# Kernel optimization log

Measured on AMD Instinct MI355X. Metric: run time of the kernel, lower is better.

Reference implementation:

```python
import jax, jax.numpy as jnp
import numpy as np

N_HEADS = 32
N_KV = 8
N_REP = N_HEADS // N_KV  # 4
HEAD_DIM = 128
DIM = 4096


def _rope(x, cos, sin, start_pos):
    # x: (B, H, T, hd); cos/sin: (max_seq, hd//2)
    T = x.shape[2]
    c = jax.lax.dynamic_slice_in_dim(cos, start_pos, T, axis=0)[None, None]  # (1,1,T,hd/2)
    s = jax.lax.dynamic_slice_in_dim(sin, start_pos, T, axis=0)[None, None]
    x1, x2 = x[..., : HEAD_DIM // 2], x[..., HEAD_DIM // 2:]
    return jnp.concatenate([x1 * c - x2 * s, x2 * c + x1 * s], axis=-1)


def setup_inputs() -> dict:
    key = jax.random.key(0)
    ks = jax.random.split(key, 7)
    B, T = 1, 2048
    sc = 0.02
    return {
        "x": jax.random.normal(ks[0], (B, T, DIM), jnp.float32),
        "cos": jax.random.normal(ks[1], (T, HEAD_DIM // 2), jnp.float32),
        "sin": jax.random.normal(ks[2], (T, HEAD_DIM // 2), jnp.float32),
        "wq": jax.random.normal(ks[3], (N_HEADS * HEAD_DIM, DIM), jnp.float32) * sc,
        "wk": jax.random.normal(ks[4], (N_KV * HEAD_DIM, DIM), jnp.float32) * sc,
        "wv": jax.random.normal(ks[5], (N_KV * HEAD_DIM, DIM), jnp.float32) * sc,
        "wo": jax.random.normal(ks[6], (DIM, DIM), jnp.float32) * sc,
        "start_pos": 0,
    }


def reference(x, cos, sin, wq, wk, wv, wo, start_pos):
    B, T, _ = x.shape
    # Projections (nn.Linear: y = x @ W^T)
    q = (x @ wq.T).reshape(B, T, N_HEADS, HEAD_DIM).transpose(0, 2, 1, 3)  # (B,Hq,T,hd)
    k = (x @ wk.T).reshape(B, T, N_KV, HEAD_DIM).transpose(0, 2, 1, 3)    # (B,Hk,T,hd)
    v = (x @ wv.T).reshape(B, T, N_KV, HEAD_DIM).transpose(0, 2, 1, 3)
    q = _rope(q, cos, sin, start_pos)
    k = _rope(k, cos, sin, start_pos)
    # GQA: group query heads per kv head instead of materializing repeat_kv
    qg = q.reshape(B, N_KV, N_REP, T, HEAD_DIM)
    scale = 1.0 / jnp.sqrt(jnp.float32(HEAD_DIM))
    scores = jnp.einsum('bgrqd,bgkd->bgrqk', qg, k) * scale  # (B,Hk,rep,T,T)
    causal = jnp.tril(jnp.ones((T, T), dtype=bool))
    scores = jnp.where(causal, scores, jnp.finfo(scores.dtype).min)
    attn = jax.nn.softmax(scores, axis=-1)
    yg = jnp.einsum('bgrqk,bgkd->bgrqd', attn, v)  # (B,Hk,rep,T,hd)
    y = yg.reshape(B, N_HEADS, T, HEAD_DIM).transpose(0, 2, 1, 3).reshape(B, T, DIM)
    return y @ wo.T
```

## Files before the change

### kernel.cpp

```cpp
#include <hip/hip_runtime.h>
#include <hip/hip_bf16.h>
#include <stdint.h>

using bf16 = __hip_bfloat16;
using bf16x8 = __attribute__((ext_vector_type(8))) short;
using f32x4  = __attribute__((ext_vector_type(4))) float;

#define AS1 __attribute__((address_space(1)))
#define AS3 __attribute__((address_space(3)))

__device__ __forceinline__ void async_ld16(const void* g, void* l) {
    __builtin_amdgcn_global_load_lds((const AS1 void*)g, (AS3 void*)l, 16, 0, 0);
}

__device__ __forceinline__ f32x4 mfma_bf16(bf16x8 a, bf16x8 b, f32x4 c) {
    return __builtin_amdgcn_mfma_f32_16x16x32_bf16(a, b, c, 0, 0, 0);
}

__device__ __forceinline__ float sexp(float x) {
    return __expf(fmaxf(x, -80.0f));
}

template<int N> __device__ __forceinline__ float dpp_max16(float x) {
    int xi = __builtin_bit_cast(int, x);
    int yi = __builtin_amdgcn_update_dpp(xi, xi, 0x110 | N, 0xf, 0xf, false);
    return fmaxf(x, __builtin_bit_cast(float, yi));
}
template<int N> __device__ __forceinline__ float dpp_add16(float x) {
    int xi = __builtin_bit_cast(int, x);
    int yi = __builtin_amdgcn_update_dpp(0, xi, 0x110 | N, 0xf, 0xf, true);
    return x + __builtin_bit_cast(float, yi);
}
__device__ __forceinline__ float bcast15(float x) {
    return __builtin_bit_cast(float,
        __builtin_amdgcn_ds_swizzle(__builtin_bit_cast(int, x), 0x01F0));
}
__device__ __forceinline__ float redmax16(float x) {
    x = dpp_max16<1>(x); x = dpp_max16<2>(x);
    x = dpp_max16<4>(x); x = dpp_max16<8>(x);
    return bcast15(x);
}
__device__ __forceinline__ float redsum16(float x) {
    x = dpp_add16<1>(x); x = dpp_add16<2>(x);
    x = dpp_add16<4>(x); x = dpp_add16<8>(x);
    return bcast15(x);
}

__device__ __forceinline__ void cvt8(const float* p, bf16* d) {
    float4 lo = *(const float4*)p;
    float4 hi = *(const float4*)(p + 4);
    bf16 t8[8] = {__float2bfloat16(lo.x), __float2bfloat16(lo.y),
                  __float2bfloat16(lo.z), __float2bfloat16(lo.w),
                  __float2bfloat16(hi.x), __float2bfloat16(hi.y),
                  __float2bfloat16(hi.z), __float2bfloat16(hi.w)};
    *(bf16x8*)d = *(const bf16x8*)t8;
}

__global__ __launch_bounds__(256) void cvt4_k(const float* __restrict__ x,  bf16* __restrict__ xb,
                                              const float* __restrict__ wq, bf16* __restrict__ wqb,
                                              const float* __restrict__ wk, bf16* __restrict__ wkb,
                                              const float* __restrict__ wv, bf16* __restrict__ wvb) {
    int stride = gridDim.x * blockDim.x;
    for (int u = blockIdx.x * blockDim.x + threadIdx.x; u < 4194304; u += stride) {
        const float* s; bf16* d; size_t off;
        if (u < 1048576)      { s = x;  d = xb;  off = (size_t)u * 8; }
        else if (u < 3145728) { s = wq; d = wqb; off = (size_t)(u - 1048576) * 8; }
        else if (u < 3670016) { s = wk; d = wkb; off = (size_t)(u - 3145728) * 8; }
        else                  { s = wv; d = wvb; off = (size_t)(u - 3670016) * 8; }
        cvt8(s + off, d + off);
    }
}

__global__ __launch_bounds__(256) void cvt_f32_bf16(const float* __restrict__ src,
                                                    bf16* __restrict__ dst, int n8) {
    int stride = gridDim.x * blockDim.x;
    for (int u = blockIdx.x * blockDim.x + threadIdx.x; u < n8; u += stride)
        cvt8(src + (size_t)u * 8, dst + (size_t)u * 8);
}

template<bool SRCF32>
__device__ __forceinline__ void stage_tile(const void* __restrict__ src,
                                           bf16* __restrict__ s,
                                           int row0, int K, int k0, int tid) {
    if constexpr (SRCF32) {
        const float* g = (const float*)src;
        #pragma unroll
        for (int i = 0; i < 2; ++i) {
            int u = tid + 256 * i;
            int row = u >> 2, c8 = (u & 3) * 8;
            cvt8(g + (size_t)(row0 + row) * K + k0 + c8, &s[row * 32 + c8]);
        }
    } else {
        const bf16* g = (const bf16*)src;
        const int wave = tid >> 6, lane = tid & 63;
        const int c0 = wave * 64 + lane;
        const int r0 = c0 >> 2, cb0 = (c0 & 3) * 16;
        const int c1 = 256 + c0;
        const int r1 = c1 >> 2, cb1 = (c1 & 3) * 16;
        async_ld16((const char*)(g + (size_t)(row0 + r0) * K + k0) + cb0,
                   (char*)s + wave * 1024);
        async_ld16((const char*)(g + (size_t)(row0 + r1) * K + k0) + cb1,
                   (char*)s + 4096 + wave * 1024);
    }
}

template<bool AF32, bool BF32, int MODE>
__global__ __launch_bounds__(256) void gemm_bt(const void* __restrict__ A,
                                               const void* __restrict__ B,
                                               void* __restrict__ C,
                                               bf16* __restrict__ Qp,
                                               bf16* __restrict__ Kp,
                                               bf16* __restrict__ Vp,
                                               int M, int N, int K) {
    __shared__ bf16 sA[128 * 32];
    __shared__ bf16 sB[128 * 32];
    const int tid  = threadIdx.x;
    const int lane = tid & 63;
    const int wave = tid >> 6;
    const int m0 = blockIdx.y * 128;
    const int n0 = blockIdx.x * 128;
    const int mrow = (wave >> 1) * 64;
    const int ncol = (wave & 1) * 64;

    f32x4 acc[4][4] = {};

    for (int k0 = 0; k0 < K; k0 += 32) {
        __syncthreads();
        stage_tile<AF32>(A, sA, m0, K, k0, tid);
        stage_tile<BF32>(B, sB, n0, K, k0, tid);
        __syncthreads();

        bf16x8 af[4], bfr[4];
        #pragma unroll
        for (int i = 0; i < 4; ++i)
            af[i] = *(const bf16x8*)&sA[(mrow + i * 16 + (lane & 15)) * 32 + (lane >> 4) * 8];
        #pragma unroll
        for (int j = 0; j < 4; ++j)
            bfr[j] = *(const bf16x8*)&sB[(ncol + j * 16 + (lane & 15)) * 32 + (lane >> 4) * 8];
        #pragma unroll
        for (int i = 0; i < 4; ++i)
            #pragma unroll
            for (int j = 0; j < 4; ++j)
                acc[i][j] = mfma_bf16(af[i], bfr[j], acc[i][j]);
    }

    #pragma unroll
    for (int i = 0; i < 4; ++i)
        #pragma unroll
        for (int j = 0; j < 4; ++j)
            #pragma unroll
            for (int r = 0; r < 4; ++r) {
                int row = m0 + mrow + i * 16 + (lane >> 4) * 4 + r;
                int col = n0 + ncol + j * 16 + (lane & 15);
                float fv = acc[i][j][r];
                if constexpr (MODE == 0) {
                    ((bf16*)C)[(size_t)row * N + col] = __float2bfloat16(fv);
                } else if constexpr (MODE == 1) {
                    ((bf16*)C)[(size_t)col * M + row] = __float2bfloat16(fv);
                } else if constexpr (MODE == 2) {
                    bf16 v = __float2bfloat16(fv);
                    if (col < 4096)      Qp[(size_t)row * 4096 + col] = v;
                    else if (col < 5120) Kp[(size_t)row * 1024 + (col - 4096)] = v;
                    else                 Vp[(size_t)(col - 5120) * 2048 + row] = v;
                } else {
                    ((float*)C)[(size_t)row * N + col] = fv;
                }
            }
}

__global__ __launch_bounds__(256) void rope_all(bf16* __restrict__ Q,
                                                bf16* __restrict__ K,
                                                const float* __restrict__ cosp,
                                                const float* __restrict__ sinp,
                                                const int* __restrict__ spp) {
    int idx = blockIdx.x * blockDim.x + threadIdx.x;
    int d = idx & 63;
    int h = (idx >> 6) % 40;
    int t = idx / (64 * 40);
    int sp = *spp;
    float c = cosp[(size_t)(t + sp) * 64 + d];
    float s = sinp[(size_t)(t + sp) * 64 + d];
    bf16* row = (h < 32) ? (Q + (size_t)t * 4096 + h * 128)
                         : (K + (size_t)t * 1024 + (h - 32) * 128);
    float x1 = __bfloat162float(row[d]);
    float x2 = __bfloat162float(row[64 + d]);
    row[d]      = __float2bfloat16(x1 * c - x2 * s);
    row[64 + d] = __float2bfloat16(x2 * c + x1 * s);
}

#define NEG_SENT (-1.0e9f)
__global__ __launch_bounds__(256) void attn_k(const bf16* __restrict__ Q,
                                              const bf16* __restrict__ K,
                                              const bf16* __restrict__ VT,
                                              bf16* __restrict__ Y) {
    constexpr int SKS = 136;
    constexpr int SVS = 72;
    __shared__ bf16 sK[64 * SKS];
    __shared__ bf16 sVT[128 * SVS];

    const int tid  = threadIdx.x;
    const int lane = tid & 63;
    const int wave = tid >> 6;
    const int qtile = 31 - (blockIdx.x >> 5);
    const int head  = blockIdx.x & 31;
    const int g     = head >> 2;
    const int qrow0 = qtile * 64 + wave * 16;
    bf16* sPw = sK + wave * 1152;

    bf16x8 qf[4];
    {
        const bf16* qbase = Q + (size_t)(qrow0 + (lane & 15)) * 4096 + head * 128;
        #pragma unroll
        for (int kk = 0; kk < 4; ++kk)
            qf[kk] = *(const bf16x8*)(qbase + kk * 32 + (lane >> 4) * 8);
    }

    float m_i[4], l_i[4];
    #pragma unroll
    for (int r = 0; r < 4; ++r) { m_i[r] = NEG_SENT; l_i[r] = 0.f; }
    f32x4 o[8] = {};
    const float scale = 0.08838834764831845f;

    for (int kt = 0; kt <= qtile; ++kt) {
        const int kt0 = kt * 64;
        __syncthreads();
        #pragma unroll
        for (int i = 0; i < 4; ++i) {
            int c = i * 256 + tid;
            {
                int row = c >> 4, ch = c & 15;
                *(uint4*)&sK[row * SKS + ch * 8] =
                    *(const uint4*)(K + (size_t)(kt0 + row) * 1024 + g * 128 + ch * 8);
            }
            {
                int row = c >> 3, ch = c & 7;
                *(uint4*)&sVT[row * SVS + ch * 8] =
                    *(const uint4*)(VT + (size_t)(g * 128 + row) * 2048 + kt0 + ch * 8);
            }
        }
        __syncthreads();

        f32x4 s[4];
        #pragma unroll
        for (int j = 0; j < 4; ++j) {
            f32x4 a = {};
            #pragma unroll
            for (int kk = 0; kk < 4; ++kk) {
                bf16x8 kfrag = *(const bf16x8*)&sK[(j * 16 + (lane & 15)) * SKS +
                                                   kk * 32 + (lane >> 4) * 8];
                a = mfma_bf16(qf[kk], kfrag, a);
            }
            s[j] = a;
        }

        #pragma unroll
        for (int j = 0; j < 4; ++j) {
            int tk = kt0 + j * 16 + (lane & 15);
            #pragma unroll
            for (int r = 0; r < 4; ++r) {
                int tq = qrow0 + (lane >> 4) * 4 + r;
                float v = s[j][r] * scale;
                s[j][r] = (tk > tq) ? NEG_SENT : v;
            }
        }

        #pragma unroll
        for (int r = 0; r < 4; ++r) {
            float mx = fmaxf(fmaxf(s[0][r], s[1][r]), fmaxf(s[2][r], s[3][r]));
            mx = redmax16(mx);
            float mn = fmaxf(m_i[r], mx);
            float alpha = sexp(m_i[r] - mn);
            m_i[r] = mn;
            float rs = 0.f;
            #pragma unroll
            for (int j = 0; j < 4; ++j) {
                float pv = sexp(s[j][r] - mn);
                s[j][r] = pv;
                rs += pv;
            }
            l_i[r] = l_i[r] * alpha + rs;
            #pragma unroll
            for (int j2 = 0; j2 < 8; ++j2) o[j2][r] *= alpha;
        }

        __syncthreads();

        #pragma unroll
        for (int j = 0; j < 4; ++j)
            #pragma unroll
            for (int r = 0; r < 4; ++r)
                sPw[((lane >> 4) * 4 + r) * SVS + j * 16 + (lane & 15)] =
                    __float2bfloat16(s[j][r]);
        __asm__ volatile("s_waitcnt lgkmcnt(0)" ::: "memory");

        #pragma unroll
        for (int kk2 = 0; kk2 < 2; ++kk2) {
            bf16x8 pf = *(const bf16x8*)&sPw[(lane & 15) * SVS + kk2 * 32 + (lane >> 4) * 8];
            #pragma unroll
            for (int j2 = 0; j2 < 8; ++j2) {
                bf16x8 vf = *(const bf16x8*)&sVT[(j2 * 16 + (lane & 15)) * SVS +
                                                 kk2 * 32 + (lane >> 4) * 8];
                o[j2] = mfma_bf16(pf, vf, o[j2]);
            }
        }
    }

    #pragma unroll
    for (int r = 0; r < 4; ++r) l_i[r] = redsum16(l_i[r]);
    #pragma unroll
    for (int j2 = 0; j2 < 8; ++j2)
        #pragma unroll
        for (int r = 0; r < 4; ++r) {
            int t   = qrow0 + (lane >> 4) * 4 + r;
            int col = head * 128 + j2 * 16 + (lane & 15);
            Y[(size_t)t * 4096 + col] = __float2bfloat16(o[j2][r] / l_i[r]);
        }
}

extern "C" void kernel_launch(void* const* d_in, const int* in_sizes, int n_in,
                              void* d_out, int out_size, void* d_ws, size_t ws_size,
                              hipStream_t stream) {
    const float* x    = (const float*)d_in[0];
    const float* cosp = (const float*)d_in[1];
    const float* sinp = (const float*)d_in[2];
    const float* wq   = (const float*)d_in[3];
    const float* wk   = (const float*)d_in[4];
    const float* wv   = (const float*)d_in[5];
    const float* wo   = (const float*)d_in[6];
    const int*   sp   = (const int*)d_in[7];
    float* out = (float*)d_out;

    char* ws = (char*)d_ws;
    bf16* Qb = (bf16*)d_out;

    const size_t NEED = 92274688;
    if (ws_size >= NEED) {
        bf16* xb   = (bf16*)(ws);
        bf16* wqkv = (bf16*)(ws + (16u << 20));
        bf16* wob  = wqkv;
        bf16* Kb   = (bf16*)(ws + (64u << 20));
        bf16* VT   = (bf16*)(ws + (68u << 20));
        bf16* Yb   = (bf16*)(ws + (72u << 20));

        cvt4_k<<<dim3(4096), 256, 0, stream>>>(x, xb, wq, wqkv,
                                               wk, wqkv + 16777216, wv, wqkv + 20971520);

        gemm_bt<false, false, 2><<<dim3(48, 16), 256, 0, stream>>>(
            xb, wqkv, nullptr, Qb, Kb, VT, 2048, 6144, 4096);

        cvt_f32_bf16<<<dim3(4096), 256, 0, stream>>>(wo, wob, 2097152);

        rope_all<<<dim3(2048 * 40 * 64 / 256), 256, 0, stream>>>(Qb, Kb, cosp, sinp, sp);

        attn_k<<<dim3(1024), 256, 0, stream>>>(Qb, Kb, VT, Yb);

        gemm_bt<false, false, 3><<<dim3(32, 16), 256, 0, stream>>>(
            Yb, wob, out, nullptr, nullptr, nullptr, 2048, 4096, 4096);
    } else {
        bf16* Kb = (bf16*)(ws);
        bf16* VT = (bf16*)(ws + (4u << 20));
        bf16* Yb = (bf16*)(ws + (8u << 20));

        gemm_bt<true, true, 0><<<dim3(32, 16), 256, 0, stream>>>(
            x, wq, Qb, nullptr, nullptr, nullptr, 2048, 4096, 4096);
        gemm_bt<true, true, 0><<<dim3(8, 16), 256, 0, stream>>>(
            x, wk, Kb, nullptr, nullptr, nullptr, 2048, 1024, 4096);
        gemm_bt<true, true, 1><<<dim3(8, 16), 256, 0, stream>>>(
            x, wv, VT, nullptr, nullptr, nullptr, 2048, 1024, 4096);

        rope_all<<<dim3(2048 * 40 * 64 / 256), 256, 0, stream>>>(Qb, Kb, cosp, sinp, sp);

        attn_k<<<dim3(1024), 256, 0, stream>>>(Qb, Kb, VT, Yb);

        gemm_bt<false, true, 3><<<dim3(32, 16), 256, 0, stream>>>(
            Yb, wo, out, nullptr, nullptr, nullptr, 2048, 4096, 4096);
    }
}
```

Measured before the change: 542.4 us.

## Add 4-stage async-LDS pipelined bf16 GEMM for QKV and output projections

Adds a new GEMM kernel, gemm_bt_p, that keeps four LDS buffers and issues global_load_lds prefetches three k-tiles ahead. Each step does a single barrier, raises wave priority around the MFMA block, and uses an XOR-swizzled LDS layout. Both the QKV and output projections in the workspace path now use it. The aim is to hide global-memory latency behind MFMA work. In exchange it uses 64KB of LDS per block, which limits occupancy, and its tail iterations issue redundant loads of k-tile 0.

```diff
diff --git a/kernel.cpp b/kernel.cpp
--- a/kernel.cpp
+++ b/kernel.cpp
@@ -158,6 +158,117 @@
                 } else if constexpr (MODE == 1) {
                     ((bf16*)C)[(size_t)col * M + row] = __float2bfloat16(fv);
                 } else if constexpr (MODE == 2) {
+                    bf16 v = __float2bfloat16(fv);
+                    if (col < 4096)      Qp[(size_t)row * 4096 + col] = v;
+                    else if (col < 5120) Kp[(size_t)row * 1024 + (col - 4096)] = v;
+                    else                 Vp[(size_t)(col - 5120) * 2048 + row] = v;
+                } else {
+                    ((float*)C)[(size_t)row * N + col] = fv;
+                }
+            }
+}
+
+template<int MODE>
+__global__ __launch_bounds__(256, 2) void gemm_bt_p(const bf16* __restrict__ A,
+                                                    const bf16* __restrict__ B,
+                                                    void* __restrict__ C,
+                                                    bf16* __restrict__ Qp,
+                                                    bf16* __restrict__ Kp,
+                                                    bf16* __restrict__ Vp,
+                                                    int M, int N, int K) {
+    __shared__ __align__(16) bf16 s0[8192];
+    __shared__ __align__(16) bf16 s1[8192];
+    __shared__ __align__(16) bf16 s2[8192];
+    __shared__ __align__(16) bf16 s3[8192];
+
+    const int tid  = threadIdx.x;
+    const int lane = tid & 63;
+    const int wave = tid >> 6;
+    const int m0 = blockIdx.y * 128;
+    const int n0 = blockIdx.x * 128;
+    const int mrow = (wave >> 1) * 64;
+    const int ncol = (wave & 1) * 64;
+    const int NT = K >> 5;
+
+    int offA[4], offB[4];
+    {
+        const int q = lane >> 4;
+        #pragma unroll
+        for (int i = 0; i < 4; ++i) {
+            const int ra = mrow + i * 16 + (lane & 15);
+            offA[i] = ra * 32 + ((q ^ ((ra >> 1) & 3)) * 8);
+            const int rb = ncol + i * 16 + (lane & 15);
+            offB[i] = rb * 32 + ((q ^ ((rb >> 1) & 3)) * 8);
+        }
+    }
+
+    const int u0  = wave * 64 + lane, u1 = u0 + 256;
+    const int rA0 = u0 >> 2, q0 = (u0 & 3) ^ ((rA0 >> 1) & 3);
+    const int rA1 = u1 >> 2, q1 = (u1 & 3) ^ ((rA1 >> 1) & 3);
+    const bf16* gA0 = A + (size_t)(m0 + rA0) * K + q0 * 8;
+    const bf16* gA1 = A + (size_t)(m0 + rA1) * K + q1 * 8;
+    const bf16* gB0 = B + (size_t)(n0 + rA0) * K + q0 * 8;
+    const bf16* gB1 = B + (size_t)(n0 + rA1) * K + q1 * 8;
+    const int d0 = wave * 512;
+    const int d1 = 2048 + wave * 512;
+
+    auto stage = [&](bf16* dst, int k0) __attribute__((always_inline)) {
+        async_ld16(gA0 + k0, dst + d0);
+        async_ld16(gA1 + k0, dst + d1);
+        async_ld16(gB0 + k0, dst + 4096 + d0);
+        async_ld16(gB1 + k0, dst + 4096 + d1);
+    };
+
+    f32x4 acc[4][4] = {};
+
+    stage(s0, 0);
+    stage(s1, 32);
+    stage(s2, 64);
+    asm volatile("s_waitcnt vmcnt(8)" ::: "memory");
+    __builtin_amdgcn_s_barrier();
+    asm volatile("" ::: "memory");
+    __builtin_amdgcn_sched_barrier(0);
+
+    auto body = [&](const bf16* sCur, bf16* sNxt, int t) __attribute__((always_inline)) {
+        bf16x8 af[4], bfr[4];
+        #pragma unroll
+        for (int i = 0; i < 4; ++i) af[i]  = *(const bf16x8*)(sCur + offA[i]);
+        #pragma unroll
+        for (int j = 0; j < 4; ++j) bfr[j] = *(const bf16x8*)(sCur + 4096 + offB[j]);
+        const int k3 = (t + 3 < NT) ? (t + 3) * 32 : 0;
+        stage(sNxt, k3);
+        __builtin_amdgcn_s_setprio(1);
+        #pragma unroll
+        for (int i = 0; i < 4; ++i)
+            #pragma unroll
+            for (int j = 0; j < 4; ++j)
+                acc[i][j] = mfma_bf16(af[i], bfr[j], acc[i][j]);
+        __builtin_amdgcn_s_setprio(0);
+        __builtin_amdgcn_sched_barrier(0);
+        asm volatile("s_waitcnt vmcnt(8) lgkmcnt(0)" ::: "memory");
+        __builtin_amdgcn_s_barrier();
+        asm volatile("" ::: "memory");
+        __builtin_amdgcn_sched_barrier(0);
+    };
+
+    for (int t = 0; t < NT; t += 4) {
+        body(s0, s3, t);
+        body(s1, s0, t + 1);
+        body(s2, s1, t + 2);
+        body(s3, s2, t + 3);
+    }
+    asm volatile("s_waitcnt vmcnt(0)" ::: "memory");
+
+    #pragma unroll
+    for (int i = 0; i < 4; ++i)
+        #pragma unroll
+        for (int j = 0; j < 4; ++j)
+            #pragma unroll
+            for (int r = 0; r < 4; ++r) {
+                int row = m0 + mrow + i * 16 + (lane >> 4) * 4 + r;
+                int col = n0 + ncol + j * 16 + (lane & 15);
+                float fv = acc[i][j][r];
+                if constexpr (MODE == 2) {
                     bf16 v = __float2bfloat16(fv);
                     if (col < 4096)      Qp[(size_t)row * 4096 + col] = v;
                     else if (col < 5120) Kp[(size_t)row * 1024 + (col - 4096)] = v;
@@ -345,7 +456,7 @@
         cvt4_k<<<dim3(4096), 256, 0, stream>>>(x, xb, wq, wqkv,
                                                wk, wqkv + 16777216, wv, wqkv + 20971520);
 
-        gemm_bt<false, false, 2><<<dim3(48, 16), 256, 0, stream>>>(
+        gemm_bt_p<2><<<dim3(48, 16), 256, 0, stream>>>(
             xb, wqkv, nullptr, Qb, Kb, VT, 2048, 6144, 4096);
 
         cvt_f32_bf16<<<dim3(4096), 256, 0, stream>>>(wo, wob, 2097152);
@@ -354,7 +465,7 @@
 
         attn_k<<<dim3(1024), 256, 0, stream>>>(Qb, Kb, VT, Yb);
 
-        gemm_bt<false, false, 3><<<dim3(32, 16), 256, 0, stream>>>(
+        gemm_bt_p<3><<<dim3(32, 16), 256, 0, stream>>>(
             Yb, wob, out, nullptr, nullptr, nullptr, 2048, 4096, 4096);
     } else {
         bf16* Kb = (bf16*)(ws);
```

Result: faster. 504.4 us (-7.0%).

## Add 8-wave triple-buffered 256x128 GEMM with phased async LDS loads

Applied to the files above, without the earlier changes.

Adds a new bf16 GEMM kernel using 512 threads (8 waves), 256x128 block tiles, triple-buffered LDS filled via global_load_lds, XOR-swizzled layout, and a four-phase schedule that interleaves staging loads with MFMA work under barriers and raised priority. The QKV projection and output projection in the workspace path switch to this kernel. It aims to hide global-memory latency and raise MFMA utilisation. The larger tile halves the number of blocks, which may reduce wave occupancy and load balance across CUs.

```diff
diff --git a/kernel.cpp b/kernel.cpp
--- a/kernel.cpp
+++ b/kernel.cpp
@@ -158,6 +158,140 @@
                 } else if constexpr (MODE == 1) {
                     ((bf16*)C)[(size_t)col * M + row] = __float2bfloat16(fv);
                 } else if constexpr (MODE == 2) {
+                    bf16 v = __float2bfloat16(fv);
+                    if (col < 4096)      Qp[(size_t)row * 4096 + col] = v;
+                    else if (col < 5120) Kp[(size_t)row * 1024 + (col - 4096)] = v;
+                    else                 Vp[(size_t)(col - 5120) * 2048 + row] = v;
+                } else {
+                    ((float*)C)[(size_t)row * N + col] = fv;
+                }
+            }
+}
+
+#define VMW(N) asm volatile("s_waitcnt vmcnt(" #N ")" ::: "memory")
+
+#define PH(SA, SB, MH, NH, STG, WT) do {                                          \
+    bf16x8 aF[2][2], bF[2][2];                                                    \
+    _Pragma("unroll") for (int i2 = 0; i2 < 2; ++i2)                              \
+      _Pragma("unroll") for (int kh = 0; kh < 2; ++kh)                            \
+        aF[i2][kh] = *(const bf16x8*)((SA) + offA[(MH)*2 + i2][kh]);              \
+    _Pragma("unroll") for (int j2 = 0; j2 < 2; ++j2)                              \
+      _Pragma("unroll") for (int kh = 0; kh < 2; ++kh)                            \
+        bF[j2][kh] = *(const bf16x8*)((SB) + offB[(NH)*2 + j2][kh]);              \
+    STG;                                                                          \
+    __builtin_amdgcn_s_barrier();                                                 \
+    asm volatile("s_waitcnt lgkmcnt(0)" ::: "memory");                            \
+    __builtin_amdgcn_sched_barrier(0);                                            \
+    __builtin_amdgcn_s_setprio(1);                                                \
+    _Pragma("unroll") for (int i2 = 0; i2 < 2; ++i2)                              \
+      _Pragma("unroll") for (int j2 = 0; j2 < 2; ++j2)                            \
+        _Pragma("unroll") for (int kh = 0; kh < 2; ++kh)                          \
+          acc[(MH)*2 + i2][(NH)*2 + j2] =                                         \
+              mfma_bf16(aF[i2][kh], bF[j2][kh], acc[(MH)*2 + i2][(NH)*2 + j2]);   \
+    __builtin_amdgcn_s_setprio(0);                                                \
+    __builtin_amdgcn_sched_barrier(0);                                            \
+    WT;                                                                           \
+    __builtin_amdgcn_s_barrier();                                                 \
+  } while (0)
+
+#define TILE(SA, SB, SA2, SB2, T2, DOST, WT) do {                                 \
+    PH(SA, SB, 0, 0, if (DOST) stgA01(SA2, T2), );                                \
+    PH(SA, SB, 0, 1, if (DOST) stgA23(SA2, T2), );                                \
+    PH(SA, SB, 1, 0, if (DOST) stgB0(SB2, T2), );                                 \
+    PH(SA, SB, 1, 1, if (DOST) stgB1(SB2, T2), WT);                               \
+  } while (0)
+
+template<int MODE>
+__global__ __launch_bounds__(512, 1) void gemm_8p(const bf16* __restrict__ A,
+                                                  const bf16* __restrict__ B,
+                                                  void* __restrict__ C,
+                                                  bf16* __restrict__ Qp,
+                                                  bf16* __restrict__ Kp,
+                                                  bf16* __restrict__ Vp,
+                                                  int M, int N, int K) {
+    __shared__ __align__(16) bf16 sA0[16384], sA1[16384], sA2[16384];
+    __shared__ __align__(16) bf16 sB0[8192],  sB1[8192],  sB2[8192];
+
+    const int tid  = threadIdx.x;
+    const int lane = tid & 63;
+    const int wave = tid >> 6;
+    const int wr   = wave >> 1;
+    const int wc   = wave & 1;
+    const int m0 = blockIdx.y * 256;
+    const int n0 = blockIdx.x * 128;
+    const int NT = K >> 6;
+
+    int offA[4][2], offB[4][2];
+    {
+        const int l15 = lane & 15, l4 = lane >> 4;
+        #pragma unroll
+        for (int i = 0; i < 4; ++i) {
+            const int ra = wr * 64 + i * 16 + l15;
+            const int rb = wc * 64 + i * 16 + l15;
+            #pragma unroll
+            for (int kh = 0; kh < 2; ++kh) {
+                offA[i][kh] = ra * 64 + (((kh * 4 + l4) ^ (ra & 7)) * 8);
+                offB[i][kh] = rb * 64 + (((kh * 4 + l4) ^ (rb & 7)) * 8);
+            }
+        }
+    }
+
+    const int rloc = tid >> 3;
+    const int qsw  = (tid & 7) ^ (rloc & 7);
+    const bf16* gA0 = A + (size_t)(m0 +   0 + rloc) * K + qsw * 8;
+    const bf16* gA1 = A + (size_t)(m0 +  64 + rloc) * K + qsw * 8;
+    const bf16* gA2 = A + (size_t)(m0 + 128 + rloc) * K + qsw * 8;
+    const bf16* gA3 = A + (size_t)(m0 + 192 + rloc) * K + qsw * 8;
+    const bf16* gB0 = B + (size_t)(n0 +   0 + rloc) * K + qsw * 8;
+    const bf16* gB1 = B + (size_t)(n0 +  64 + rloc) * K + qsw * 8;
+    const int w512 = wave * 512;
+
+    auto stgA01 = [&](bf16* dst, int kt) __attribute__((always_inline)) {
+        async_ld16(gA0 + kt * 64, dst + w512);
+        async_ld16(gA1 + kt * 64, dst + 4096 + w512);
+    };
+    auto stgA23 = [&](bf16* dst, int kt) __attribute__((always_inline)) {
+        async_ld16(gA2 + kt * 64, dst + 8192 + w512);
+        async_ld16(gA3 + kt * 64, dst + 12288 + w512);
+    };
+    auto stgB0 = [&](bf16* dst, int kt) __attribute__((always_inline)) {
+        async_ld16(gB0 + kt * 64, dst + w512);
+    };
+    auto stgB1 = [&](bf16* dst, int kt) __attribute__((always_inline)) {
+        async_ld16(gB1 + kt * 64, dst + 4096 + w512);
+    };
+
+    f32x4 acc[4][4] = {};
+
+    stgA01(sA0, 0); stgA23(sA0, 0); stgB0(sB0, 0); stgB1(sB0, 0);
+    stgA01(sA1, 1); stgA23(sA1, 1); stgB0(sB1, 1); stgB1(sB1, 1);
+    VMW(6);
+    __builtin_amdgcn_s_barrier();
+    asm volatile("" ::: "memory");
+    __builtin_amdgcn_sched_barrier(0);
+
+    int t = 0;
+    for (; t < NT - 6; t += 3) {
+        TILE(sA0, sB0, sA2, sB2, t + 2, true, VMW(6));
+        TILE(sA1, sB1, sA0, sB0, t + 3, true, VMW(6));
+        TILE(sA2, sB2, sA1, sB1, t + 4, true, VMW(6));
+    }
+    TILE(sA0, sB0, sA2, sB2, NT - 2, true,  VMW(6));
+    TILE(sA1, sB1, sA0, sB0, NT - 1, true,  VMW(6));
+    TILE(sA2, sB2, sA0, sB0, 0,      false, VMW(0));
+    TILE(sA0, sB0, sA1, sB1, 0,      false, );
+    asm volatile("s_waitcnt vmcnt(0)" ::: "memory");
+
+    #pragma unroll
+    for (int i = 0; i < 4; ++i)
+        #pragma unroll
+        for (int j = 0; j < 4; ++j)
+            #pragma unroll
+            for (int r = 0; r < 4; ++r) {
+                int row = m0 + wr * 64 + i * 16 + (lane >> 4) * 4 + r;
+                int col = n0 + wc * 64 + j * 16 + (lane & 15);
+                float fv = acc[i][j][r];
+                if constexpr (MODE == 2) {
                     bf16 v = __float2bfloat16(fv);
                     if (col < 4096)      Qp[(size_t)row * 4096 + col] = v;
                     else if (col < 5120) Kp[(size_t)row * 1024 + (col - 4096)] = v;
@@ -345,7 +479,7 @@
         cvt4_k<<<dim3(4096), 256, 0, stream>>>(x, xb, wq, wqkv,
                                                wk, wqkv + 16777216, wv, wqkv + 20971520);
 
-        gemm_bt<false, false, 2><<<dim3(48, 16), 256, 0, stream>>>(
+        gemm_8p<2><<<dim3(48, 8), 512, 0, stream>>>(
             xb, wqkv, nullptr, Qb, Kb, VT, 2048, 6144, 4096);
 
         cvt_f32_bf16<<<dim3(4096), 256, 0, stream>>>(wo, wob, 2097152);
@@ -354,7 +488,7 @@
 
         attn_k<<<dim3(1024), 256, 0, stream>>>(Qb, Kb, VT, Yb);
 
-        gemm_bt<false, false, 3><<<dim3(32, 16), 256, 0, stream>>>(
+        gemm_8p<3><<<dim3(32, 8), 512, 0, stream>>>(
             Yb, wob, out, nullptr, nullptr, nullptr, 2048, 4096, 4096);
     } else {
         bf16* Kb = (bf16*)(ws);
```

Result: slower. 568.6 us (+4.8%).
